# Kernel tuning notes

Measured on AMD Instinct MI355X. Metric: run time of the kernel, lower is better.

Reference implementation:

```python
import jax, jax.numpy as jnp
import numpy as np


def setup_inputs() -> dict:
    key = jax.random.key(0)
    k0, k1 = jax.random.split(key)
    B, C, H, W = 8, 16, 512, 512
    im0 = jax.random.normal(k0, (B, C, H, W), dtype=jnp.float32)
    flow = jax.random.normal(k1, (B, H, W, 2), dtype=jnp.float32)
    im1 = jnp.zeros((B, C, H, W), dtype=jnp.float32)
    return {"im0": im0, "flow": flow, "im1": im1}


def _forward_warp_bilinear(im0, flow, im1):
    # im0: [B,C,H,W], flow: [B,H,W,2] (flow[...,0]=dx, flow[...,1]=dy), im1: [B,C,H,W]
    B, C, H, W = im0.shape
    gx = jnp.arange(W, dtype=flow.dtype)[None, None, :]   # [1,1,W]
    gy = jnp.arange(H, dtype=flow.dtype)[None, :, None]   # [1,H,1]
    x = gx + flow[..., 0]                                 # [B,H,W] dest x
    y = gy + flow[..., 1]                                 # [B,H,W] dest y

    x0f = jnp.floor(x)
    y0f = jnp.floor(y)
    x0 = x0f.astype(jnp.int32)
    y0 = y0f.astype(jnp.int32)
    x1 = x0 + 1
    y1 = y0 + 1

    # Original Python/CUDA kernel scatters only if ALL four corners are in-bounds.
    valid = (x0 >= 0) & (x1 <= W - 1) & (y0 >= 0) & (y1 <= H - 1)  # [B,H,W]

    fx = x - x0f   # in [0,1)
    fy = y - y0f
    w_nw = (1.0 - fx) * (1.0 - fy)
    w_ne = fx * (1.0 - fy)
    w_sw = (1.0 - fx) * fy
    w_se = fx * fy

    # channel-last flat layout for efficient scatter: [B, H*W, C]
    src = jnp.transpose(im0, (0, 2, 3, 1)).reshape(B, H * W, C)
    out = jnp.transpose(im1, (0, 2, 3, 1)).reshape(B, H * W, C)
    bb = jnp.arange(B)[:, None]                            # [B,1] broadcasts over H*W

    for yi, xi, wgt in ((y0, x0, w_nw), (y0, x1, w_ne),
                        (y1, x0, w_sw), (y1, x1, w_se)):
        t = jnp.where(valid, yi * W + xi, 0).reshape(B, H * W)          # safe indices
        wv = jnp.where(valid, wgt, 0.0).reshape(B, H * W)               # zeroed weights
        out = out.at[bb, t].add(wv[..., None] * src)
    return jnp.transpose(out.reshape(B, H, W, C), (0, 3, 1, 2))


def reference(im0, flow, im1):
    return _forward_warp_bilinear(im0, flow, im1)
```

## Files before the change

### kernel.cpp

```cpp
#include <hip/hip_runtime.h>


#define BB 8
#define CC 16
#define HH 512
#define WW 512
#define TIL 32
#define RAD 4
#define REG (TIL + 2*RAD)
#define NSRC (REG*REG)
#define NTHR 512
#define NREC ((NSRC + NTHR - 1) / NTHR)
#define NENT (NSRC * 4)
#define CB 4
#define NGRP (CC / CB)

__global__ __launch_bounds__(NTHR, 4) void fwarp_tile(
    const float* __restrict__ im0,
    const float* __restrict__ flow,
    float* __restrict__ out)
{
    __shared__ unsigned short s_ent16[NENT];
    __shared__ float          s_wt[NENT];
    __shared__ unsigned       s_off[TIL*TIL];
    __shared__ unsigned       s_cur[TIL*TIL];
    __shared__ float4         s_img[NSRC];
    __shared__ unsigned       s_wtot[8];

    const int tid  = threadIdx.x;
    const int tile = blockIdx.x;
    const int tcx = tile & 15;
    const int tcy = (tile >> 4) & 15;
    const int b   = tile >> 8;
    const int w0  = tcx * TIL;
    const int h0  = tcy * TIL;

    const float2* flow2 = (const float2*)flow + ((size_t)b << 18);

    float4 rw[NREC];
    int    rp0[NREC];
    int    rk[NREC];

    for (int j = tid; j < TIL * TIL; j += NTHR) s_cur[j] = 0u;

#pragma unroll
    for (int r = 0; r < NREC; ++r) {
        rk[r] = 0; rp0[r] = 0;
        rw[r] = make_float4(0.f, 0.f, 0.f, 0.f);
        const int i = tid + r * NTHR;
        if (i < NSRC) {
            const int ry = i / REG;
            const int rx = i - ry * REG;
            const int sy = h0 - RAD + ry;
            const int sx = w0 - RAD + rx;
            const bool inimg = (sx >= 0) & (sx < WW) & (sy >= 0) & (sy < HH);

            float fxv = 0.0f, fyv = 0.0f;
            if (inimg) {
                const float2 f = flow2[(sy << 9) + sx];
                fxv = f.x; fyv = f.y;
            }
            const float x = (float)sx + fxv;
            const float y = (float)sy + fyv;
            const float x0f = floorf(x);
            const float y0f = floorf(y);
            const int x0 = (int)x0f;
            const int y0 = (int)y0f;

            const bool inrange = (fxv >= -(float)RAD) & (fxv < (float)RAD) &
                                 (fyv >= -(float)RAD) & (fyv < (float)RAD);
            const bool valid = inimg && inrange &&
                               (x0 >= 0) && (x0 <= WW - 2) && (y0 >= 0) && (y0 <= HH - 2);

            const float fx = x - x0f;
            const float fy = y - y0f;
            const int lx = x0 - w0;
            const int ly = y0 - h0;

            const bool okW = (lx >= 0)  & (lx < TIL);
            const bool okE = (lx >= -1) & (lx < TIL - 1);
            const bool okN = (ly >= 0)  & (ly < TIL);
            const bool okS = (ly >= -1) & (ly < TIL - 1);

            const float wnw = (1.0f - fx) * (1.0f - fy);
            const float wne = fx * (1.0f - fy);
            const float wsw = (1.0f - fx) * fy;
            const float wse = fx * fy;

            int m = 0;
            if (valid && okN && okW && (wnw != 0.0f)) m |= 1;
            if (valid && okN && okE && (wne != 0.0f)) m |= 2;
            if (valid && okS && okW && (wsw != 0.0f)) m |= 4;
            if (valid && okS && okE && (wse != 0.0f)) m |= 8;

            rk[r]  = m;
            rp0[r] = ly * TIL + lx;
            rw[r]  = make_float4(wnw, wne, wsw, wse);
        }
    }
    __syncthreads();

#pragma unroll
    for (int r = 0; r < NREC; ++r) {
        const int m = rk[r];
        const int p0 = rp0[r];
        if (m & 1) atomicAdd(&s_cur[p0], 1u);
        if (m & 2) atomicAdd(&s_cur[p0 + 1], 1u);
        if (m & 4) atomicAdd(&s_cur[p0 + TIL], 1u);
        if (m & 8) atomicAdd(&s_cur[p0 + TIL + 1], 1u);
    }
    __syncthreads();

    {
        const int lane = tid & 63;
        const int wv   = tid >> 6;
        const unsigned ca = s_cur[tid * 2 + 0];
        const unsigned cb = s_cur[tid * 2 + 1];
        const unsigned mysum = ca + cb;
        unsigned inc = mysum;
#pragma unroll
        for (int d = 1; d < 64; d <<= 1) {
            const unsigned u = __shfl_up(inc, d);
            if (lane >= d) inc += u;
        }
        if (lane == 63) s_wtot[wv] = inc;
        __syncthreads();
        unsigned wpre = 0;
#pragma unroll
        for (int w = 0; w < 7; ++w) if (wv > w) wpre += s_wtot[w];
        const unsigned o0 = wpre + inc - mysum;
        const unsigned o1 = o0 + ca;
        s_off[tid * 2 + 0] = o0;  s_cur[tid * 2 + 0] = o0;
        s_off[tid * 2 + 1] = o1;  s_cur[tid * 2 + 1] = o1;
    }
    __syncthreads();

#pragma unroll
    for (int r = 0; r < NREC; ++r) {
        const int i = tid + r * NTHR;
        const int m = rk[r];
        const int p0 = rp0[r];
        const float4 w4 = rw[r];
        if (m & 1) { const unsigned s = atomicAdd(&s_cur[p0],           1u); s_ent16[s] = (unsigned short)i; s_wt[s] = w4.x; }
        if (m & 2) { const unsigned s = atomicAdd(&s_cur[p0 + 1],       1u); s_ent16[s] = (unsigned short)i; s_wt[s] = w4.y; }
        if (m & 4) { const unsigned s = atomicAdd(&s_cur[p0 + TIL],     1u); s_ent16[s] = (unsigned short)i; s_wt[s] = w4.z; }
        if (m & 8) { const unsigned s = atomicAdd(&s_cur[p0 + TIL + 1], 1u); s_ent16[s] = (unsigned short)i; s_wt[s] = w4.w; }
    }
    __syncthreads();

    int rbeg[2], rend[2];
#pragma unroll
    for (int k = 0; k < 2; ++k) {
        const int p = tid + k * NTHR;
        rbeg[k] = (int)s_off[p];
        rend[k] = (int)s_cur[p];
    }

    const float* imb = im0 + ((size_t)(b * CC) << 18);
    float* outb      = out + ((size_t)(b * CC) << 18);

    for (int g = 0; g < NGRP; ++g) {
        const float* imgp = imb + ((size_t)(g * CB) << 18);

#pragma unroll
        for (int r = 0; r < NREC; ++r) {
            const int i = tid + r * NTHR;
            if (i < NSRC) {
                const int ry = i / REG;
                const int rx = i - ry * REG;
                const int sy = h0 - RAD + ry;
                const int sx = w0 - RAD + rx;
                const bool inimg = (sx >= 0) & (sx < WW) & (sy >= 0) & (sy < HH);
                const int gi = inimg ? ((sy << 9) + sx) : 0;
                float4 v;
                v.x = imgp[gi];
                v.y = imgp[((size_t)1 << 18) + gi];
                v.z = imgp[((size_t)2 << 18) + gi];
                v.w = imgp[((size_t)3 << 18) + gi];
                s_img[i] = v;
            }
        }
        __syncthreads();

#pragma unroll
        for (int k = 0; k < 2; ++k) {
            const int p   = tid + k * NTHR;
            const int beg = rbeg[k];
            const int end = rend[k];

            float a0 = 0.f, a1 = 0.f, a2 = 0.f, a3 = 0.f;
            for (int j = beg; j < end; ++j) {
                const int   sp = (int)s_ent16[j];
                const float w  = s_wt[j];
                const float4 v = s_img[sp];
                a0 = fmaf(w, v.x, a0);
                a1 = fmaf(w, v.y, a1);
                a2 = fmaf(w, v.z, a2);
                a3 = fmaf(w, v.w, a3);
            }

            const int dy = p >> 5;
            const int dx = p & 31;
            float* op = outb + ((size_t)(g * CB) << 18) + ((h0 + dy) << 9) + (w0 + dx);
            op[0]                 = a0;
            op[(size_t)1 << 18]   = a1;
            op[(size_t)2 << 18]   = a2;
            op[(size_t)3 << 18]   = a3;
        }
        __syncthreads();
    }
}

__global__ __launch_bounds__(256) void fwarp_fallback(
    const float* __restrict__ im0,
    const float* __restrict__ flow,
    float* __restrict__ out)
{
    const int t = blockIdx.x * blockDim.x + threadIdx.x;
    const int idx0 = t << 2;

    const float4 fA = ((const float4*)flow)[(t << 1)];
    const float4 fB = ((const float4*)flow)[(t << 1) + 1];
    const float pfx[4] = {fA.x, fA.z, fB.x, fB.z};
    const float pfy[4] = {fA.y, fA.w, fB.y, fB.w};

#pragma unroll
    for (int k = 0; k < 4; ++k) {
        const float fxv = pfx[k];
        const float fyv = pfy[k];
        const bool inrange = (fxv >= -(float)RAD) & (fxv < (float)RAD) &
                             (fyv >= -(float)RAD) & (fyv < (float)RAD);
        if (inrange) continue;

        const int idx = idx0 + k;
        const int w = idx & (WW - 1);
        const int h = (idx >> 9) & (HH - 1);
        const int b = idx >> 18;

        const float x = (float)w + fxv;
        const float y = (float)h + fyv;
        const float x0f = floorf(x);
        const float y0f = floorf(y);
        const int x0 = (int)x0f;
        const int y0 = (int)y0f;
        if (x0 < 0 || x0 > WW - 2 || y0 < 0 || y0 > HH - 2) continue;

        const float fx = x - x0f;
        const float fy = y - y0f;
        const float wnw = (1.0f - fx) * (1.0f - fy);
        const float wne = fx * (1.0f - fy);
        const float wsw = (1.0f - fx) * fy;
        const float wse = fx * fy;

        const size_t plane = (size_t)HH * WW;
        const float* srcb = im0 + (size_t)b * CC * plane + (size_t)h * WW + w;
        float* dstb       = out + (size_t)b * CC * plane;
        const int o = y0 * WW + x0;

#pragma unroll
        for (int c = 0; c < CC; ++c) {
            const float v = srcb[c * plane];
            float* dc = dstb + c * plane;
            atomicAdd(dc + o,          v * wnw);
            atomicAdd(dc + o + 1,      v * wne);
            atomicAdd(dc + o + WW,     v * wsw);
            atomicAdd(dc + o + WW + 1, v * wse);
        }
    }
}

extern "C" void kernel_launch(void* const* d_in, const int* in_sizes, int n_in,
                              void* d_out, int out_size, void* d_ws, size_t ws_size,
                              hipStream_t stream) {
    const float* im0  = (const float*)d_in[0];
    const float* flow = (const float*)d_in[1];
    float* out = (float*)d_out;

    const int n_tiles = BB * (HH / TIL) * (WW / TIL);
    fwarp_tile<<<n_tiles, NTHR, 0, stream>>>(im0, flow, out);

    const int n_pix = BB * HH * WW;
    fwarp_fallback<<<n_pix / (256 * 4), 256, 0, stream>>>(im0, flow, out);
}
```

Baseline: 354.6 us.

## Quantize weights to 16-bit, shrink channel group, prefetch image into registers

Result: faster. 327.0 us (-7.8%).

```diff
diff --git a/kernel.cpp b/kernel.cpp
--- a/kernel.cpp
+++ b/kernel.cpp
@@ -12,23 +12,22 @@
 #define NTHR 512
 #define NREC ((NSRC + NTHR - 1) / NTHR)
 #define NENT (NSRC * 4)
-#define CB 4
+#define CB 2
 #define NGRP (CC / CB)
 
-__global__ __launch_bounds__(NTHR, 4) void fwarp_tile(
+__global__ __launch_bounds__(NTHR, 6) void fwarp_tile(
     const float* __restrict__ im0,
     const float* __restrict__ flow,
     float* __restrict__ out)
 {
-    __shared__ unsigned short s_ent16[NENT];
-    __shared__ float          s_wt[NENT];
-    __shared__ unsigned       s_off[TIL*TIL];
-    __shared__ unsigned       s_cur[TIL*TIL];
-    __shared__ float4         s_img[NSRC];
-    __shared__ unsigned       s_wtot[8];
-
-    const int tid  = threadIdx.x;
-    const int tile = blockIdx.x;
+    __shared__ unsigned s_ent[NENT];
+    __shared__ unsigned s_cur[TIL * TIL];
+    __shared__ float2   s_img[NSRC];
+    __shared__ unsigned s_wtot[8];
+
+    const int tid = threadIdx.x;
+    const int bid  = blockIdx.x;
+    const int tile = ((bid & 7) << 8) | (bid >> 3);
     const int tcx = tile & 15;
     const int tcy = (tile >> 4) & 15;
     const int b   = tile >> 8;
@@ -40,12 +39,13 @@
     float4 rw[NREC];
     int    rp0[NREC];
     int    rk[NREC];
+    int    rgi[NREC];
 
     for (int j = tid; j < TIL * TIL; j += NTHR) s_cur[j] = 0u;
 
 #pragma unroll
     for (int r = 0; r < NREC; ++r) {
-        rk[r] = 0; rp0[r] = 0;
+        rk[r] = 0; rp0[r] = 0; rgi[r] = 0;
         rw[r] = make_float4(0.f, 0.f, 0.f, 0.f);
         const int i = tid + r * NTHR;
         if (i < NSRC) {
@@ -54,6 +54,7 @@
             const int sy = h0 - RAD + ry;
             const int sx = w0 - RAD + rx;
             const bool inimg = (sx >= 0) & (sx < WW) & (sy >= 0) & (sy < HH);
+            rgi[r] = inimg ? ((sy << 9) + sx) : 0;
 
             float fxv = 0.0f, fyv = 0.0f;
             if (inimg) {
@@ -130,9 +131,14 @@
         for (int w = 0; w < 7; ++w) if (wv > w) wpre += s_wtot[w];
         const unsigned o0 = wpre + inc - mysum;
         const unsigned o1 = o0 + ca;
-        s_off[tid * 2 + 0] = o0;  s_cur[tid * 2 + 0] = o0;
-        s_off[tid * 2 + 1] = o1;  s_cur[tid * 2 + 1] = o1;
-    }
+        s_cur[tid * 2 + 0] = o0;
+        s_cur[tid * 2 + 1] = o1;
+    }
+    __syncthreads();
+
+    int rbeg[2], rend[2];
+#pragma unroll
+    for (int k = 0; k < 2; ++k) rbeg[k] = (int)s_cur[tid + k * NTHR];
     __syncthreads();
 
 #pragma unroll
@@ -141,46 +147,52 @@
         const int m = rk[r];
         const int p0 = rp0[r];
         const float4 w4 = rw[r];
-        if (m & 1) { const unsigned s = atomicAdd(&s_cur[p0],           1u); s_ent16[s] = (unsigned short)i; s_wt[s] = w4.x; }
-        if (m & 2) { const unsigned s = atomicAdd(&s_cur[p0 + 1],       1u); s_ent16[s] = (unsigned short)i; s_wt[s] = w4.y; }
-        if (m & 4) { const unsigned s = atomicAdd(&s_cur[p0 + TIL],     1u); s_ent16[s] = (unsigned short)i; s_wt[s] = w4.z; }
-        if (m & 8) { const unsigned s = atomicAdd(&s_cur[p0 + TIL + 1], 1u); s_ent16[s] = (unsigned short)i; s_wt[s] = w4.w; }
-    }
-    __syncthreads();
-
-    int rbeg[2], rend[2];
-#pragma unroll
-    for (int k = 0; k < 2; ++k) {
-        const int p = tid + k * NTHR;
-        rbeg[k] = (int)s_off[p];
-        rend[k] = (int)s_cur[p];
-    }
+        if (m & 1) { const unsigned s = atomicAdd(&s_cur[p0],           1u);
+                     s_ent[s] = ((unsigned)i << 16) | (unsigned)(w4.x * 65535.0f + 0.5f); }
+        if (m & 2) { const unsigned s = atomicAdd(&s_cur[p0 + 1],       1u);
+                     s_ent[s] = ((unsigned)i << 16) | (unsigned)(w4.y * 65535.0f + 0.5f); }
+        if (m & 4) { const unsigned s = atomicAdd(&s_cur[p0 + TIL],     1u);
+                     s_ent[s] = ((unsigned)i << 16) | (unsigned)(w4.z * 65535.0f + 0.5f); }
+        if (m & 8) { const unsigned s = atomicAdd(&s_cur[p0 + TIL + 1], 1u);
+                     s_ent[s] = ((unsigned)i << 16) | (unsigned)(w4.w * 65535.0f + 0.5f); }
+    }
+    __syncthreads();
+#pragma unroll
+    for (int k = 0; k < 2; ++k) rend[k] = (int)s_cur[tid + k * NTHR];
 
     const float* imb = im0 + ((size_t)(b * CC) << 18);
     float* outb      = out + ((size_t)(b * CC) << 18);
 
-    for (int g = 0; g < NGRP; ++g) {
-        const float* imgp = imb + ((size_t)(g * CB) << 18);
-
+    float2 vimg[NREC];
+
+    {
+        const float* p0c = imb;
+        const float* p1c = imb + ((size_t)1 << 18);
 #pragma unroll
         for (int r = 0; r < NREC; ++r) {
             const int i = tid + r * NTHR;
-            if (i < NSRC) {
-                const int ry = i / REG;
-                const int rx = i - ry * REG;
-                const int sy = h0 - RAD + ry;
-                const int sx = w0 - RAD + rx;
-                const bool inimg = (sx >= 0) & (sx < WW) & (sy >= 0) & (sy < HH);
-                const int gi = inimg ? ((sy << 9) + sx) : 0;
-                float4 v;
-                v.x = imgp[gi];
-                v.y = imgp[((size_t)1 << 18) + gi];
-                v.z = imgp[((size_t)2 << 18) + gi];
-                v.w = imgp[((size_t)3 << 18) + gi];
-                s_img[i] = v;
+            if (i < NSRC) { vimg[r].x = p0c[rgi[r]]; vimg[r].y = p1c[rgi[r]]; }
+        }
+    }
+
+    for (int g = 0; g < NGRP; ++g) {
+        __syncthreads();
+#pragma unroll
+        for (int r = 0; r < NREC; ++r) {
+            const int i = tid + r * NTHR;
+            if (i < NSRC) s_img[i] = vimg[r];
+        }
+        __syncthreads();
+
+        if (g + 1 < NGRP) {
+            const float* p0c = imb + ((size_t)((g + 1) * CB) << 18);
+            const float* p1c = imb + ((size_t)((g + 1) * CB + 1) << 18);
+#pragma unroll
+            for (int r = 0; r < NREC; ++r) {
+                const int i = tid + r * NTHR;
+                if (i < NSRC) { vimg[r].x = p0c[rgi[r]]; vimg[r].y = p1c[rgi[r]]; }
             }
         }
-        __syncthreads();
 
 #pragma unroll
         for (int k = 0; k < 2; ++k) {
@@ -188,26 +200,22 @@
             const int beg = rbeg[k];
             const int end = rend[k];
 
-            float a0 = 0.f, a1 = 0.f, a2 = 0.f, a3 = 0.f;
+            float a0 = 0.f, a1 = 0.f;
             for (int j = beg; j < end; ++j) {
-                const int   sp = (int)s_ent16[j];
-                const float w  = s_wt[j];
-                const float4 v = s_img[sp];
+                const unsigned e = s_ent[j];
+                const int   sp = (int)(e >> 16);
+                const float w  = (float)(e & 0xFFFFu) * (1.0f / 65535.0f);
+                const float2 v = s_img[sp];
                 a0 = fmaf(w, v.x, a0);
                 a1 = fmaf(w, v.y, a1);
-                a2 = fmaf(w, v.z, a2);
-                a3 = fmaf(w, v.w, a3);
             }
 
             const int dy = p >> 5;
             const int dx = p & 31;
             float* op = outb + ((size_t)(g * CB) << 18) + ((h0 + dy) << 9) + (w0 + dx);
-            op[0]                 = a0;
-            op[(size_t)1 << 18]   = a1;
-            op[(size_t)2 << 18]   = a2;
-            op[(size_t)3 << 18]   = a3;
-        }
-        __syncthreads();
+            op[0]               = a0;
+            op[(size_t)1 << 18] = a1;
+        }
     }
 }
 
```
